# Performance work log

Measured on AMD Instinct MI355X. Metric: run time of the kernel, lower is better.

Reference implementation:

```python
import jax, jax.numpy as jnp
import numpy as np

B, T, F = 512, 256, 64
H = [128, 256, 128, 64]

def _glorot(key, shape):
    fan_in, fan_out = shape[0], shape[1]
    lim = np.sqrt(6.0 / (fan_in + fan_out))
    return jax.random.uniform(key, shape, jnp.float32, -lim, lim)

def setup_inputs() -> dict:
    key = jax.random.key(0)
    ks = jax.random.split(key, 16)
    inp = {"x": jax.random.normal(ks[0], (B, T, F), jnp.float32)}
    dims = [F] + H
    for i in range(4):
        inp[f"Wx{i+1}"] = _glorot(ks[1 + 3 * i], (dims[i], dims[i + 1]))
        # keras uses orthogonal recurrent init; scaled normal is an acceptable stand-in
        q, _ = jnp.linalg.qr(jax.random.normal(ks[2 + 3 * i], (dims[i + 1], dims[i + 1])))
        inp[f"Wh{i+1}"] = q.astype(jnp.float32)
        inp[f"b{i+1}"] = jnp.zeros((dims[i + 1],), jnp.float32)
    inp["Wd"] = _glorot(ks[13], (T * H[-1], 1))
    inp["bd"] = jnp.zeros((1,), jnp.float32)
    return inp

def simple_rnn(x, Wx, Wh, b):
    # x: [B, T, Fin] -> hidden sequence [B, T, H]; h_t = relu(x_t Wx + h_{t-1} Wh + b)
    xp = jnp.einsum('btf,fh->tbh', x, Wx) + b  # precompute input projection, time-major
    h0 = jnp.zeros((x.shape[0], Wh.shape[0]), x.dtype)
    def step(h, xt):
        h = jax.nn.relu(xt + h @ Wh)
        return h, h
    _, hs = jax.lax.scan(step, h0, xp)  # hs: [T, B, H]
    return jnp.transpose(hs, (1, 0, 2))

def reference(x, Wx1, Wh1, b1, Wx2, Wh2, b2, Wx3, Wh3, b3, Wx4, Wh4, b4, Wd, bd):
    h = simple_rnn(x, Wx1, Wh1, b1)   # dropout layers are identity at inference
    h = simple_rnn(h, Wx2, Wh2, b2)
    h = simple_rnn(h, Wx3, Wh3, b3)
    h = simple_rnn(h, Wx4, Wh4, b4)
    flat = h.reshape(h.shape[0], -1)  # [B, T*64]
    return flat @ Wd + bd             # [B, 1]
```

## Files before the change

kernel.cpp:

```cpp
#include <hip/hip_runtime.h>
#include <hip/hip_bf16.h>

#define BB 512
#define TT 256

typedef __attribute__((ext_vector_type(8))) short bf16x8;
typedef __attribute__((ext_vector_type(4))) float f32x4;

__device__ __forceinline__ unsigned short f2b(float f) {
    union { float f; unsigned u; } v; v.f = f;
    unsigned r = v.u + 0x7FFFu + ((v.u >> 16) & 1u);
    return (unsigned short)(r >> 16);
}
__device__ __forceinline__ float b2f(unsigned short h) {
    union { unsigned u; float f; } v; v.u = ((unsigned)h) << 16;
    return v.f;
}
__device__ __forceinline__ ushort2 pk2(float a, float b) {
    __hip_bfloat162 h = __float22bfloat162_rn(float2{a, b});
    union { __hip_bfloat162 h; ushort2 u; } v; v.h = h; return v.u;
}


__global__ __launch_bounds__(256) void cvt_tile(const float* __restrict__ x,
                                                unsigned short* __restrict__ xb) {
    const int blk = blockIdx.x;
    const int s = blk >> 8, t = blk & 255;
    const int tid = threadIdx.x;
    const int b = (tid >> 1) & 15;
    const int f0 = (tid >> 5) * 8 + (tid & 1) * 4;
    float4 v = *reinterpret_cast<const float4*>(
        &x[(((size_t)(s * 16 + b) * TT) + t) * 64 + f0]);
    ushort2 lo = pk2(v.x, v.y), hi = pk2(v.z, v.w);
    ushort4 o; o.x = lo.x; o.y = lo.y; o.z = hi.x; o.w = hi.y;
    *reinterpret_cast<ushort4*>(&xb[(size_t)blk * 1024 + tid * 4]) = o;
}

__global__ __launch_bounds__(512) __attribute__((amdgpu_waves_per_eu(2, 2))) void rnn4(
    const unsigned short* __restrict__ Xb,
    const float* __restrict__ Wx1, const float* __restrict__ Wh1, const float* __restrict__ b1,
    const float* __restrict__ Wx2, const float* __restrict__ Wh2, const float* __restrict__ b2,
    const float* __restrict__ Wx3, const float* __restrict__ Wh3, const float* __restrict__ b3,
    const float* __restrict__ Wx4, const float* __restrict__ Wh4, const float* __restrict__ b4,
    unsigned short* __restrict__ H4) {
    const int tid = threadIdx.x;
    const int s = blockIdx.x;
    const int w = tid >> 6;
    const int lane = tid & 63;
    const int l15 = lane & 15;
    const int quad = lane >> 4;
    const int rdo = quad * 128 + l15 * 8;

    __shared__ __align__(16) unsigned short hall[2][9216];

    bf16x8 wreg[48];
    f32x4 bvv[6];

#define LOADW(BASE, WP, H_, CB, KC_, MT_)                                          \
    _Pragma("unroll")                                                              \
    for (int mt = 0; mt < MT_; ++mt) {                                             \
        int m = (CB) + mt * 16 + l15;                                              \
        _Pragma("unroll")                                                          \
        for (int kc = 0; kc < KC_; ++kc)                                           \
            _Pragma("unroll")                                                      \
            for (int j = 0; j < 8; ++j)                                            \
                wreg[(BASE) + kc * MT_ + mt][j] =                                  \
                    (short)f2b(WP[(kc * 32 + quad * 8 + j) * H_ + m]);             \
    }
#define LOADBF(OFF, BP, CB, MT_)                                                   \
    _Pragma("unroll")                                                              \
    for (int mt = 0; mt < MT_; ++mt) {                                             \
        float4 t4v = *reinterpret_cast<const float4*>((BP) + (CB) + mt * 16 + quad * 4); \
        bvv[(OFF) + mt][0] = t4v.x; bvv[(OFF) + mt][1] = t4v.y;                    \
        bvv[(OFF) + mt][2] = t4v.z; bvv[(OFF) + mt][3] = t4v.w;                    \
    }

    if (w < 2) {
        LOADW(0,  Wh1, 128, w * 64, 4, 4)
        LOADW(16, Wx1, 128, w * 64, 2, 4)
        LOADW(24, Wh4, 64,  w * 32, 2, 2)
        LOADW(28, Wx4, 64,  w * 32, 4, 2)
        LOADBF(0, b1, w * 64, 4)
        LOADBF(4, b4, w * 32, 2)
    } else if (w < 6) {
        LOADW(0,  Wh2, 256, (w - 2) * 64, 8, 4)
        LOADW(32, Wx2, 256, (w - 2) * 64, 4, 4)
        LOADBF(0, b2, (w - 2) * 64, 4)
    } else {
        LOADW(0,  Wh3, 128, (w - 6) * 64, 4, 4)
        LOADW(16, Wx3, 128, (w - 6) * 64, 8, 4)
        LOADBF(0, b3, (w - 6) * 64, 4)
    }
#undef LOADW
#undef LOADBF

    for (int i = tid; i < 2 * 9216; i += 512) (&hall[0][0])[i] = 0;

    const unsigned short* Xs = Xb + (size_t)s * TT * 1024;
    unsigned short* H4s = H4 + (size_t)s * TT * 1024;

    if (w < 2) {
#pragma unroll
        for (int kx = 0; kx < 2; ++kx) {
            wreg[36 + kx] = *reinterpret_cast<const bf16x8*>(&Xs[kx * 512 + rdo]);
            wreg[38 + kx] = *reinterpret_cast<const bf16x8*>(&Xs[1024 + kx * 512 + rdo]);
        }
    }
    __syncthreads();

    const unsigned short* xp0 = Xs + 2 * 1024 + rdo;
    const unsigned short* xp1 = Xs + 3 * 1024 + rdo;

    const int wro1 = (w * 8 + (quad >> 1)) * 128 + l15 * 8 + (quad & 1) * 4;
    const int wro4 = 8192 + (w * 4 + (quad >> 1)) * 128 + l15 * 8 + (quad & 1) * 4;
    const int wro2 = 2048 + ((w - 2) * 8 + (quad >> 1)) * 128 + l15 * 8 + (quad & 1) * 4;
    const int wro3 = 6144 + ((w - 6) * 8 + (quad >> 1)) * 128 + l15 * 8 + (quad & 1) * 4;

    unsigned short* op_e = H4s + 1024 + (wro4 - 8192);
    unsigned short* op_o = H4s + (wro4 - 8192);

#define PACKMK(ACC_MT)                                                             \
    ushort2 lo = pk2(fmaxf((ACC_MT)[0], 0.f), fmaxf((ACC_MT)[1], 0.f));            \
    ushort2 hi = pk2(fmaxf((ACC_MT)[2], 0.f), fmaxf((ACC_MT)[3], 0.f));            \
    ushort4 o; o.x = lo.x; o.y = lo.y; o.z = hi.x; o.w = hi.y;

#define STEP(TAU_, RP_, WP_, XAB, XPP, OPP)                                        \
    {                                                                              \
        const int tau_ = (TAU_);                                                   \
        const unsigned short* RB = &hall[RP_][0];                                  \
        unsigned short* WB = &hall[WP_][0];                                        \
        if (w < 2) {                                                               \
            if ((unsigned)tau_ < TT) {                                     \
                f32x4 acc[4];                                                      \
                _Pragma("unroll")                                                  \
                for (int mt = 0; mt < 4; ++mt)                                     \
                    acc[mt] = __builtin_amdgcn_mfma_f32_16x16x32_bf16(             \
                        wreg[16 + mt], wreg[(XAB) + 0], bvv[mt], 0, 0, 0);         \
                _Pragma("unroll")                                                  \
                for (int mt = 0; mt < 4; ++mt)                                     \
                    acc[mt] = __builtin_amdgcn_mfma_f32_16x16x32_bf16(             \
                        wreg[20 + mt], wreg[(XAB) + 1], acc[mt], 0, 0, 0);         \
                if (tau_ + 2 < TT) {                                               \
                    wreg[(XAB) + 0] = *reinterpret_cast<const bf16x8*>(XPP);       \
                    wreg[(XAB) + 1] = *reinterpret_cast<const bf16x8*>(XPP + 512); \
                    XPP += 2048;                                                   \
                }                                                                  \
                _Pragma("unroll")                                                  \
                for (int kc = 0; kc < 4; ++kc) {                                   \
                    bf16x8 af = *reinterpret_cast<const bf16x8*>(&RB[rdo + kc * 512]); \
                    _Pragma("unroll")                                              \
                    for (int mt = 0; mt < 4; ++mt)                                 \
                        acc[mt] = __builtin_amdgcn_mfma_f32_16x16x32_bf16(         \
                            wreg[kc * 4 + mt], af, acc[mt], 0, 0, 0);              \
                }                                                                  \
                _Pragma("unroll")                                                  \
                for (int mt = 0; mt < 4; ++mt) {                                   \
                    PACKMK(acc[mt])                                                \
                    *reinterpret_cast<ushort4*>(&WB[wro1 + mt * 256]) = o;         \
                }                                                                  \
            }                                                                      \
            if ((unsigned)(tau_ - 3) < TT) {                               \
                f32x4 acc[2];                                                      \
                {                                                                  \
                    bf16x8 af0 = *reinterpret_cast<const bf16x8*>(&RB[6144 + rdo]); \
                    _Pragma("unroll")                                              \
                    for (int mt = 0; mt < 2; ++mt)                                 \
                        acc[mt] = __builtin_amdgcn_mfma_f32_16x16x32_bf16(         \
                            wreg[28 + mt], af0, bvv[4 + mt], 0, 0, 0);             \
                }                                                                  \
                _Pragma("unroll")                                                  \
                for (int kx = 1; kx < 4; ++kx) {                                   \
                    bf16x8 af = *reinterpret_cast<const bf16x8*>(&RB[6144 + rdo + kx * 512]); \
                    _Pragma("unroll")                                              \
                    for (int mt = 0; mt < 2; ++mt)                                 \
                        acc[mt] = __builtin_amdgcn_mfma_f32_16x16x32_bf16(         \
                            wreg[28 + kx * 2 + mt], af, acc[mt], 0, 0, 0);         \
                }                                                                  \
                _Pragma("unroll")                                                  \
                for (int kc = 0; kc < 2; ++kc) {                                   \
                    bf16x8 af = *reinterpret_cast<const bf16x8*>(&RB[8192 + rdo + kc * 512]); \
                    _Pragma("unroll")                                              \
                    for (int mt = 0; mt < 2; ++mt)                                 \
                        acc[mt] = __builtin_amdgcn_mfma_f32_16x16x32_bf16(         \
                            wreg[24 + kc * 2 + mt], af, acc[mt], 0, 0, 0);         \
                }                                                                  \
                _Pragma("unroll")                                                  \
                for (int mt = 0; mt < 2; ++mt) {                                   \
                    PACKMK(acc[mt])                                                \
                    *reinterpret_cast<ushort4*>(&WB[wro4 + mt * 256]) = o;         \
                    *reinterpret_cast<ushort4*>(OPP + mt * 256) = o;               \
                }                                                                  \
                OPP += 2048;                                                       \
            }                                                                      \
        } else if (w < 6) {                                                        \
            if ((unsigned)(tau_ - 1) < TT) {                               \
                f32x4 acc[4];                                                      \
                {                                                                  \
                    bf16x8 af0 = *reinterpret_cast<const bf16x8*>(&RB[rdo]);       \
                    _Pragma("unroll")                                              \
                    for (int mt = 0; mt < 4; ++mt)                                 \
                        acc[mt] = __builtin_amdgcn_mfma_f32_16x16x32_bf16(         \
                            wreg[32 + mt], af0, bvv[mt], 0, 0, 0);                 \
                }                                                                  \
                _Pragma("unroll")                                                  \
                for (int kx = 1; kx < 4; ++kx) {                                   \
                    bf16x8 af = *reinterpret_cast<const bf16x8*>(&RB[rdo + kx * 512]); \
                    _Pragma("unroll")                                              \
                    for (int mt = 0; mt < 4; ++mt)                                 \
                        acc[mt] = __builtin_amdgcn_mfma_f32_16x16x32_bf16(         \
                            wreg[32 + kx * 4 + mt], af, acc[mt], 0, 0, 0);         \
                }                                                                  \
                _Pragma("unroll")                                                  \
                for (int kc = 0; kc < 8; ++kc) {                                   \
                    bf16x8 af = *reinterpret_cast<const bf16x8*>(&RB[2048 + rdo + kc * 512]); \
                    _Pragma("unroll")                                              \
                    for (int mt = 0; mt < 4; ++mt)                                 \
                        acc[mt] = __builtin_amdgcn_mfma_f32_16x16x32_bf16(         \
                            wreg[kc * 4 + mt], af, acc[mt], 0, 0, 0);              \
                }                                                                  \
                _Pragma("unroll")                                                  \
                for (int mt = 0; mt < 4; ++mt) {                                   \
                    PACKMK(acc[mt])                                                \
                    *reinterpret_cast<ushort4*>(&WB[wro2 + mt * 256]) = o;         \
                }                                                                  \
            }                                                                      \
        } else {                                                                   \
            if ((unsigned)(tau_ - 2) < TT) {                               \
                f32x4 acc[4];                                                      \
                {                                                                  \
                    bf16x8 af0 = *reinterpret_cast<const bf16x8*>(&RB[2048 + rdo]); \
                    _Pragma("unroll")                                              \
                    for (int mt = 0; mt < 4; ++mt)                                 \
                        acc[mt] = __builtin_amdgcn_mfma_f32_16x16x32_bf16(         \
                            wreg[16 + mt], af0, bvv[mt], 0, 0, 0);                 \
                }                                                                  \
                _Pragma("unroll")                                                  \
                for (int kx = 1; kx < 8; ++kx) {                                   \
                    bf16x8 af = *reinterpret_cast<const bf16x8*>(&RB[2048 + rdo + kx * 512]); \
                    _Pragma("unroll")                                              \
                    for (int mt = 0; mt < 4; ++mt)                                 \
                        acc[mt] = __builtin_amdgcn_mfma_f32_16x16x32_bf16(         \
                            wreg[16 + kx * 4 + mt], af, acc[mt], 0, 0, 0);         \
                }                                                                  \
                _Pragma("unroll")                                                  \
                for (int kc = 0; kc < 4; ++kc) {                                   \
                    bf16x8 af = *reinterpret_cast<const bf16x8*>(&RB[6144 + rdo + kc * 512]); \
                    _Pragma("unroll")                                              \
                    for (int mt = 0; mt < 4; ++mt)                                 \
                        acc[mt] = __builtin_amdgcn_mfma_f32_16x16x32_bf16(         \
                            wreg[kc * 4 + mt], af, acc[mt], 0, 0, 0);              \
                }                                                                  \
                _Pragma("unroll")                                                  \
                for (int mt = 0; mt < 4; ++mt) {                                   \
                    PACKMK(acc[mt])                                                \
                    *reinterpret_cast<ushort4*>(&WB[wro3 + mt * 256]) = o;         \
                }                                                                  \
            }                                                                      \
        }                                                                          \
        __builtin_amdgcn_s_waitcnt(0xC07F);                                        \
        __builtin_amdgcn_s_barrier();                                              \
    }

#pragma unroll 1
    for (int tau = 0; tau < TT + 3; tau += 2) {
        STEP(tau, 0, 1, 36, xp0, op_e)
        STEP(tau + 1, 1, 0, 38, xp1, op_o)
    }
#undef STEP
#undef PACKMK
}

__global__ __launch_bounds__(256) void dense_kernel(const unsigned short* __restrict__ Ht,
                                                    const float* __restrict__ Wd,
                                                    const float* __restrict__ bd,
                                                    float* __restrict__ out) {
    __shared__ float red[16][17];
    const int s = blockIdx.x;
    const int tid = threadIdx.x;
    const int b = (tid >> 1) & 15;
    const int kbase = (tid >> 5) * 8 + (tid & 1) * 4;
    const unsigned short* base = Ht + (size_t)s * TT * 1024 + tid * 4;
    float acc = 0.f;
    for (int t = 0; t < TT; ++t) {
        ushort4 v = *reinterpret_cast<const ushort4*>(base + (size_t)t * 1024);
        const float* wd = &Wd[t * 64 + kbase];
        acc += b2f(v.x) * wd[0] + b2f(v.y) * wd[1] + b2f(v.z) * wd[2] + b2f(v.w) * wd[3];
    }
    red[b][(tid >> 5) * 2 + (tid & 1)] = acc;
    __syncthreads();
    if (tid < 16) {
        float sum = 0.f;
#pragma unroll
        for (int j = 0; j < 16; ++j) sum += red[tid][j];
        out[s * 16 + tid] = sum + bd[0];
    }
}

extern "C" void kernel_launch(void* const* d_in, const int* in_sizes, int n_in,
                              void* d_out, int out_size, void* d_ws, size_t ws_size,
                              hipStream_t stream) {
    (void)in_sizes; (void)n_in; (void)out_size; (void)ws_size;
    const float* x   = (const float*)d_in[0];
    const float* Wx1 = (const float*)d_in[1];
    const float* Wh1 = (const float*)d_in[2];
    const float* b1  = (const float*)d_in[3];
    const float* Wx2 = (const float*)d_in[4];
    const float* Wh2 = (const float*)d_in[5];
    const float* b2  = (const float*)d_in[6];
    const float* Wx3 = (const float*)d_in[7];
    const float* Wh3 = (const float*)d_in[8];
    const float* b3  = (const float*)d_in[9];
    const float* Wx4 = (const float*)d_in[10];
    const float* Wh4 = (const float*)d_in[11];
    const float* b4  = (const float*)d_in[12];
    const float* Wd  = (const float*)d_in[13];
    const float* bd  = (const float*)d_in[14];
    float* out = (float*)d_out;

    char* ws = (char*)d_ws;
    unsigned short* xbT = (unsigned short*)(ws);
    unsigned short* H4  = (unsigned short*)(ws + 16777216);

    cvt_tile<<<8192, 256, 0, stream>>>(x, xbT);

    rnn4<<<32, 512, 0, stream>>>(xbT, Wx1, Wh1, b1, Wx2, Wh2, b2,
                                 Wx3, Wh3, b3, Wx4, Wh4, b4, H4);

    dense_kernel<<<32, 256, 0, stream>>>(H4, Wd, bd, out);
}
```

Measured before the change: 439.3 us.

## Fuse final dense layer into the RNN kernel and drop the H4 buffer

Layer-4 output is no longer written to a global H4 buffer for a separate dense kernel. The waves computing layer 4 now multiply their ReLU outputs by the matching Wd slice on the fly, prefetching the next timestep's Wd values. A shared-memory reduction at the end writes the output, which removes one kernel launch and the global write and read of the hidden sequence. In exchange the critical recurrent loop carries extra registers, FMAs and global loads of Wd, and the dot product now uses fp32 activations instead of bf16-rounded ones.

After: 626.4 us. +42.6%, slower.

```diff
diff --git a/kernel.cpp b/kernel.cpp
--- a/kernel.cpp
+++ b/kernel.cpp
@@ -42,7 +42,8 @@
     const float* __restrict__ Wx2, const float* __restrict__ Wh2, const float* __restrict__ b2,
     const float* __restrict__ Wx3, const float* __restrict__ Wh3, const float* __restrict__ b3,
     const float* __restrict__ Wx4, const float* __restrict__ Wh4, const float* __restrict__ b4,
-    unsigned short* __restrict__ H4) {
+    const float* __restrict__ Wd, const float* __restrict__ bd,
+    float* __restrict__ out) {
     const int tid = threadIdx.x;
     const int s = blockIdx.x;
     const int w = tid >> 6;
@@ -97,7 +98,6 @@
     for (int i = tid; i < 2 * 9216; i += 512) (&hall[0][0])[i] = 0;
 
     const unsigned short* Xs = Xb + (size_t)s * TT * 1024;
-    unsigned short* H4s = H4 + (size_t)s * TT * 1024;
 
     if (w < 2) {
 #pragma unroll
@@ -106,6 +106,23 @@
             wreg[38 + kx] = *reinterpret_cast<const bf16x8*>(&Xs[1024 + kx * 512 + rdo]);
         }
     }
+
+    f32x4 wdE[2], wdO[2], dacc[2];
+    const float* wdp_e = Wd;
+    const float* wdp_o = Wd;
+    if (w < 2) {
+        const int wco = w * 32 + quad * 4;
+#pragma unroll
+        for (int mt = 0; mt < 2; ++mt) {
+            float4 a0 = *reinterpret_cast<const float4*>(Wd + 0 * 64 + wco + mt * 16);
+            float4 a1 = *reinterpret_cast<const float4*>(Wd + 1 * 64 + wco + mt * 16);
+            wdO[mt][0] = a0.x; wdO[mt][1] = a0.y; wdO[mt][2] = a0.z; wdO[mt][3] = a0.w;
+            wdE[mt][0] = a1.x; wdE[mt][1] = a1.y; wdE[mt][2] = a1.z; wdE[mt][3] = a1.w;
+            dacc[mt] = (f32x4)(0.0f);
+        }
+        wdp_o = Wd + 2 * 64 + wco;
+        wdp_e = Wd + 3 * 64 + wco;
+    }
     __syncthreads();
 
     const unsigned short* xp0 = Xs + 2 * 1024 + rdo;
@@ -116,15 +133,12 @@
     const int wro2 = 2048 + ((w - 2) * 8 + (quad >> 1)) * 128 + l15 * 8 + (quad & 1) * 4;
     const int wro3 = 6144 + ((w - 6) * 8 + (quad >> 1)) * 128 + l15 * 8 + (quad & 1) * 4;
 
-    unsigned short* op_e = H4s + 1024 + (wro4 - 8192);
-    unsigned short* op_o = H4s + (wro4 - 8192);
-
 #define PACKMK(ACC_MT)                                                             \
     ushort2 lo = pk2(fmaxf((ACC_MT)[0], 0.f), fmaxf((ACC_MT)[1], 0.f));            \
     ushort2 hi = pk2(fmaxf((ACC_MT)[2], 0.f), fmaxf((ACC_MT)[3], 0.f));            \
     ushort4 o; o.x = lo.x; o.y = lo.y; o.z = hi.x; o.w = hi.y;
 
-#define STEP(TAU_, RP_, WP_, XAB, XPP, OPP)                                        \
+#define STEP(TAU_, RP_, WP_, XAB, XPP, WDB, WDP)                                   \
     {                                                                              \
         const int tau_ = (TAU_);                                                   \
         const unsigned short* RB = &hall[RP_][0];                                  \
@@ -159,7 +173,7 @@
                     *reinterpret_cast<ushort4*>(&WB[wro1 + mt * 256]) = o;         \
                 }                                                                  \
             }                                                                      \
-            if ((unsigned)(tau_ - 3) < TT) {                               \
+            if ((unsigned)(tau_ - 3) < TT) {                   \
                 f32x4 acc[2];                                                      \
                 {                                                                  \
                     bf16x8 af0 = *reinterpret_cast<const bf16x8*>(&RB[6144 + rdo]); \
@@ -186,11 +200,21 @@
                 }                                                                  \
                 _Pragma("unroll")                                                  \
                 for (int mt = 0; mt < 2; ++mt) {                                   \
-                    PACKMK(acc[mt])                                                \
+                    float r0 = fmaxf(acc[mt][0], 0.f), r1 = fmaxf(acc[mt][1], 0.f); \
+                    float r2 = fmaxf(acc[mt][2], 0.f), r3 = fmaxf(acc[mt][3], 0.f); \
+                    ushort2 lo = pk2(r0, r1); ushort2 hi = pk2(r2, r3);            \
+                    ushort4 o; o.x = lo.x; o.y = lo.y; o.z = hi.x; o.w = hi.y;     \
                     *reinterpret_cast<ushort4*>(&WB[wro4 + mt * 256]) = o;         \
-                    *reinterpret_cast<ushort4*>(OPP + mt * 256) = o;               \
-                }                                                                  \
-                OPP += 2048;                                                       \
+                    dacc[mt][0] += r0 * WDB[mt][0]; dacc[mt][1] += r1 * WDB[mt][1]; \
+                    dacc[mt][2] += r2 * WDB[mt][2]; dacc[mt][3] += r3 * WDB[mt][3]; \
+                }                                                                  \
+                if ((tau_ - 3) + 2 < TT) {                                         \
+                    float4 a0 = *reinterpret_cast<const float4*>(WDP);             \
+                    float4 a1 = *reinterpret_cast<const float4*>(WDP + 16);        \
+                    WDB[0][0] = a0.x; WDB[0][1] = a0.y; WDB[0][2] = a0.z; WDB[0][3] = a0.w; \
+                    WDB[1][0] = a1.x; WDB[1][1] = a1.y; WDB[1][2] = a1.z; WDB[1][3] = a1.w; \
+                    WDP += 128;                                                    \
+                }                                                                  \
             }                                                                      \
         } else if (w < 6) {                                                        \
             if ((unsigned)(tau_ - 1) < TT) {                               \
@@ -263,35 +287,23 @@
 
 #pragma unroll 1
     for (int tau = 0; tau < TT + 3; tau += 2) {
-        STEP(tau, 0, 1, 36, xp0, op_e)
-        STEP(tau + 1, 1, 0, 38, xp1, op_o)
+        STEP(tau, 0, 1, 36, xp0, wdE, wdp_e)
+        STEP(tau + 1, 1, 0, 38, xp1, wdO, wdp_o)
     }
 #undef STEP
 #undef PACKMK
-}
-
-__global__ __launch_bounds__(256) void dense_kernel(const unsigned short* __restrict__ Ht,
-                                                    const float* __restrict__ Wd,
-                                                    const float* __restrict__ bd,
-                                                    float* __restrict__ out) {
-    __shared__ float red[16][17];
-    const int s = blockIdx.x;
-    const int tid = threadIdx.x;
-    const int b = (tid >> 1) & 15;
-    const int kbase = (tid >> 5) * 8 + (tid & 1) * 4;
-    const unsigned short* base = Ht + (size_t)s * TT * 1024 + tid * 4;
-    float acc = 0.f;
-    for (int t = 0; t < TT; ++t) {
-        ushort4 v = *reinterpret_cast<const ushort4*>(base + (size_t)t * 1024);
-        const float* wd = &Wd[t * 64 + kbase];
-        acc += b2f(v.x) * wd[0] + b2f(v.y) * wd[1] + b2f(v.z) * wd[2] + b2f(v.w) * wd[3];
-    }
-    red[b][(tid >> 5) * 2 + (tid & 1)] = acc;
+
+    float* red = reinterpret_cast<float*>(&hall[0][0]);
+    if (w < 2) {
+        float p = dacc[0][0] + dacc[0][1] + dacc[0][2] + dacc[0][3]
+                + dacc[1][0] + dacc[1][1] + dacc[1][2] + dacc[1][3];
+        red[l15 * 8 + w * 4 + quad] = p;
+    }
     __syncthreads();
     if (tid < 16) {
         float sum = 0.f;
 #pragma unroll
-        for (int j = 0; j < 16; ++j) sum += red[tid][j];
+        for (int j = 0; j < 8; ++j) sum += red[tid * 8 + j];
         out[s * 16 + tid] = sum + bd[0];
     }
 }
@@ -319,12 +331,9 @@
 
     char* ws = (char*)d_ws;
     unsigned short* xbT = (unsigned short*)(ws);
-    unsigned short* H4  = (unsigned short*)(ws + 16777216);
 
     cvt_tile<<<8192, 256, 0, stream>>>(x, xbT);
 
     rnn4<<<32, 512, 0, stream>>>(xbT, Wx1, Wh1, b1, Wx2, Wh2, b2,
-                                 Wx3, Wh3, b3, Wx4, Wh4, b4, H4);
-
-    dense_kernel<<<32, 256, 0, stream>>>(H4, Wd, bd, out);
-}
+                                 Wx3, Wh3, b3, Wx4, Wh4, b4, Wd, bd, out);
+}
```
